# Kernel tuning notes

Hardware: AMD Instinct MI355X
Metric: run time of the kernel (lower is better)

## Reference

```python
import jax, jax.numpy as jnp
import numpy as np

B = 4096
HASH_BITS = 128
TEACHER_DIM = 768
TEMPERATURE = 0.2
CONTRASTIVE_W = 1.0
DISTILL_W = 0.5
QUANT_W = 0.01


def _l2_normalize(x, eps=1e-12):
    # matches torch F.normalize(dim=-1)
    n = jnp.sqrt(jnp.sum(x * x, axis=-1, keepdims=True))
    return x / jnp.maximum(n, eps)


def setup_inputs() -> dict:
    key = jax.random.key(0)
    k1, k2, k3, k4 = jax.random.split(key, 4)
    logits = jax.random.normal(k1, (B, HASH_BITS), dtype=jnp.float32)
    # binary {-1,+1} codes as in the module contract
    hash_codes = jnp.sign(jax.random.normal(k2, (B, HASH_BITS), dtype=jnp.float32))
    hash_codes = jnp.where(hash_codes == 0, 1.0, hash_codes)
    teacher_embed = jax.random.normal(k3, (B, TEACHER_DIM), dtype=jnp.float32)
    # sparse random positives plus self-positives (guarantees each row nonempty)
    rand_pos = jax.random.uniform(k4, (B, B)) < 0.002
    eye = jnp.eye(B, dtype=bool)
    positive_mask = rand_pos | eye
    return {
        "logits": logits,
        "hash_codes": hash_codes,
        "teacher_embed": teacher_embed,
        "positive_mask": positive_mask,
    }


def reference(logits, hash_codes, teacher_embed, positive_mask):
    teacher = _l2_normalize(teacher_embed)

    # ---- contrastive (vectorized form of the per-row python loop) ----
    ln = _l2_normalize(logits)
    sim = (ln @ ln.T) / TEMPERATURE  # [B, B]
    eye = jnp.eye(sim.shape[0], dtype=bool)
    sim_masked = jnp.where(eye, -jnp.inf, sim)
    # per-row stable logsumexp over self-masked similarities
    log_denom = jax.nn.logsumexp(sim_masked, axis=1)  # [B]
    pm = positive_mask.astype(sim.dtype)
    cnt = pm.sum(axis=1)  # [B]
    pos_mean = (sim * pm).sum(axis=1) / jnp.maximum(cnt, 1.0)
    has_pos = cnt > 0
    per_row = jnp.where(has_pos, -pos_mean + log_denom, 0.0)
    num_pos = jnp.maximum(has_pos.sum(), 1)
    loss_cont = per_row.sum() / num_pos.astype(sim.dtype)

    # ---- distillation: hash similarity vs teacher similarity MSE ----
    hash_sim = (hash_codes @ hash_codes.T) / hash_codes.shape[-1]
    teacher_sim = teacher @ teacher.T
    loss_distill = jnp.mean((hash_sim - teacher_sim) ** 2)

    # ---- quantization: push |logits| toward 1 ----
    loss_quant = jnp.mean(jnp.abs(jnp.abs(logits) - 1.0))

    total = (
        CONTRASTIVE_W * loss_cont
        + DISTILL_W * loss_distill
        + QUANT_W * loss_quant
    )
    return total
```

## Files before the change

### kernel.cpp

```cpp
#include <hip/hip_runtime.h>


typedef __bf16 bf16x8 __attribute__((ext_vector_type(8)));
typedef float f32x4 __attribute__((ext_vector_type(4)));

__device__ __forceinline__ unsigned short f2bf(float f) {
  union { float f; unsigned int u; } v; v.f = f;
  unsigned int u = v.u;
  return (unsigned short)((u + 0x7FFFu + ((u >> 16) & 1u)) >> 16);
}

__global__ __launch_bounds__(256) void prep(const float* __restrict__ logits,
                                            const float* __restrict__ hash,
                                            const float* __restrict__ teacher,
                                            unsigned short* __restrict__ P,
                                            unsigned char* __restrict__ Q,
                                            float* __restrict__ qpart,
                                            float* __restrict__ rowexp,
                                            float* __restrict__ possum,
                                            float* __restrict__ cntw,
                                            float* __restrict__ dtot) {
  const int r = blockIdx.x * 4 + (threadIdx.x >> 6);
  const int lane = threadIdx.x & 63;
  float2 tv[6];
  float ss = 0.f;
#pragma unroll
  for (int i = 0; i < 6; ++i) {
    tv[i] = *(const float2*)&teacher[(size_t)r * 768 + i * 128 + 2 * lane];
    ss += tv[i].x * tv[i].x + tv[i].y * tv[i].y;
  }
  const float2 lv = *(const float2*)&logits[(size_t)r * 128 + 2 * lane];
  const float2 hv = *(const float2*)&hash[(size_t)r * 128 + 2 * lane];
  float ssl = lv.x * lv.x + lv.y * lv.y;
  float qv = fabsf(fabsf(lv.x) - 1.f) + fabsf(fabsf(lv.y) - 1.f);
#pragma unroll
  for (int off = 1; off < 64; off <<= 1) {
    ss += __shfl_xor(ss, off, 64);
    ssl += __shfl_xor(ssl, off, 64);
    qv += __shfl_xor(qv, off, 64);
  }
  const float rnt = 11.313708498984761f / fmaxf(sqrtf(ss), 1e-12f);
  const float rnl = 1.f / fmaxf(sqrtf(ssl), 1e-12f);
  unsigned int pb = (unsigned int)f2bf(lv.x * rnl) |
                    ((unsigned int)f2bf(lv.y * rnl) << 16);
  *(unsigned int*)&P[(size_t)r * 128 + 2 * lane] = pb;
  unsigned short hb = (unsigned short)((hv.x >= 0.f ? 0x38 : 0xB8) |
                                       ((hv.y >= 0.f ? 0x38 : 0xB8) << 8));
  *(unsigned short*)&Q[(size_t)r * 896 + 2 * lane] = hb;
#pragma unroll
  for (int i = 0; i < 6; ++i) {
    int p = __builtin_amdgcn_cvt_pk_fp8_f32(tv[i].x * rnt, tv[i].y * rnt, 0, false);
    *(unsigned short*)&Q[(size_t)r * 896 + 128 + i * 128 + 2 * lane] =
        (unsigned short)(p & 0xFFFF);
  }
  if (lane == 0) {
    qpart[r] = qv;
    rowexp[r] = 0.f; possum[r] = 0.f; cntw[r] = 0.f;
    if (r == 0) *dtot = 0.f;
  }
}

#define STAGE_GEN(GA, GB, PITCH)                                               \
  {                                                                            \
    _Pragma("unroll") for (int it = 0; it < 4; ++it) {                         \
      const int task = it * 256 + t;                                           \
      const int row = task >> 3;                                               \
      const int c16 = (task & 7) ^ (row & 7);                                  \
      const unsigned char* gpA = (GA) + (size_t)row * (PITCH) + c16 * 16;      \
      __builtin_amdgcn_global_load_lds(                                        \
          (const __attribute__((address_space(1))) void*)gpA,                  \
          (__attribute__((address_space(3))) void*)&SB[it * 4096 + wave * 1024],\
          16, 0, 0);                                                           \
      if (offdiag) {                                                           \
        const unsigned char* gpB = (GB) + (size_t)row * (PITCH) + c16 * 16;    \
        __builtin_amdgcn_global_load_lds(                                      \
            (const __attribute__((address_space(1))) void*)gpB,                \
            (__attribute__((address_space(3)))                                 \
                 void*)&SB[16384 + it * 4096 + wave * 1024],                   \
            16, 0, 0);                                                         \
      }                                                                        \
    }                                                                          \
  }

#define MFMA_B()                                                               \
  {                                                                            \
    _Pragma("unroll") for (int ks = 0; ks < 2; ++ks) {                         \
      const int ph = ((ks * 4 + qd) ^ (l15 & 7)) * 16;                         \
      bf16x8 af[4], bfr[4];                                                    \
      _Pragma("unroll") for (int rt = 0; rt < 4; ++rt)                         \
          af[rt] = *(const bf16x8*)&SB[(wy * 64 + rt * 16 + l15) * 128 + ph];  \
      _Pragma("unroll") for (int ct = 0; ct < 4; ++ct)                         \
          bfr[ct] = *(const bf16x8*)&SB[boffB +                                \
                                        (wx * 64 + ct * 16 + l15) * 128 + ph]; \
      _Pragma("unroll") for (int rt = 0; rt < 4; ++rt)                         \
          _Pragma("unroll") for (int ct = 0; ct < 4; ++ct) acc[rt][ct] =       \
          __builtin_amdgcn_mfma_f32_16x16x32_bf16(af[rt], bfr[ct],             \
                                                  acc[rt][ct], 0, 0, 0);       \
    }                                                                          \
  }

#define MFMA_Q()                                                               \
  {                                                                            \
    _Pragma("unroll") for (int ks = 0; ks < 4; ++ks) {                         \
      const int g0 = ks * 4 + qd;                                              \
      const int ph = ((g0 >> 1) ^ (l15 & 7)) * 16 + (g0 & 1) * 8;              \
      long af[4], bfr[4];                                                      \
      _Pragma("unroll") for (int rt = 0; rt < 4; ++rt)                         \
          af[rt] = *(const long*)&SB[(wy * 64 + rt * 16 + l15) * 128 + ph];    \
      _Pragma("unroll") for (int ct = 0; ct < 4; ++ct)                         \
          bfr[ct] = *(const long*)&SB[boffB +                                  \
                                      (wx * 64 + ct * 16 + l15) * 128 + ph];   \
      _Pragma("unroll") for (int rt = 0; rt < 4; ++rt)                         \
          _Pragma("unroll") for (int ct = 0; ct < 4; ++ct) acc[rt][ct] =       \
          __builtin_amdgcn_mfma_f32_16x16x32_fp8_fp8(af[rt], bfr[ct],          \
                                                     acc[rt][ct], 0, 0, 0);    \
    }                                                                          \
  }

__global__ __launch_bounds__(256, 3) void mega(const unsigned short* __restrict__ P,
                                               const unsigned char* __restrict__ Q,
                                               const void* __restrict__ mask,
                                               float* __restrict__ rowexp,
                                               float* __restrict__ possum,
                                               float* __restrict__ cntw,
                                               float* __restrict__ dtot) {
  __shared__ __align__(16) unsigned char SB[32768];
  __shared__ float redrow[128][2], redcol[128][2], red4[4];

  const int t = threadIdx.x;
  const int wave = t >> 6, lane = t & 63;
  const int qd = lane >> 4, l15 = lane & 15;
  const int wy = wave >> 1, wx = wave & 1;

  const int b = (int)blockIdx.x;
  const bool isD = (b & 1) == 0;
  const int bb = b >> 1;
  const int l = (bb & 7) * 66 + (bb >> 3);
  int bi = (int)((65.0f - sqrtf(4225.0f - 8.0f * (float)l)) * 0.5f);
  while (bi * (65 - bi) / 2 > l) --bi;
  while ((bi + 1) * (64 - bi) / 2 <= l) ++bi;
  const int bj = bi + (l - bi * (65 - bi) / 2);
  const int ti = bi * 128, tj = bj * 128;
  const bool offdiag = (bi != bj);
  const int boffB = offdiag ? 16384 : 0;

  f32x4 acc[4][4];
#pragma unroll
  for (int rt = 0; rt < 4; ++rt)
#pragma unroll
    for (int ct = 0; ct < 4; ++ct) acc[rt][ct] = {0.f, 0.f, 0.f, 0.f};

  if (isD) {
    const unsigned char* Qa = Q + (size_t)ti * 896;
    const unsigned char* Qb = Q + (size_t)tj * 896;
    for (int kc = 0; kc < 7; ++kc) {
      const int off = (kc < 6) ? (128 + kc * 128) : 0;
      __syncthreads();
      STAGE_GEN(Qa + off, Qb + off, 896);
      __syncthreads();
      if (kc == 6) {
#pragma unroll
        for (int rt = 0; rt < 4; ++rt)
#pragma unroll
          for (int ct = 0; ct < 4; ++ct) acc[rt][ct] = -acc[rt][ct];
      }
      MFMA_Q();
    }
    float dsum = 0.f;
#pragma unroll
    for (int rt = 0; rt < 4; ++rt)
#pragma unroll
      for (int ct = 0; ct < 4; ++ct)
#pragma unroll
        for (int i = 0; i < 4; ++i) dsum += acc[rt][ct][i] * acc[rt][ct][i];
#pragma unroll
    for (int off = 1; off < 64; off <<= 1) dsum += __shfl_xor(dsum, off, 64);
    if (lane == 0) red4[wave] = dsum;
    __syncthreads();
    if (t == 0)
      atomicAdd(dtot, (offdiag ? 2.0f : 1.0f) *
                          (red4[0] + red4[1] + red4[2] + red4[3]));
  } else {
    const unsigned char* Pa = (const unsigned char*)(P + (size_t)ti * 128);
    const unsigned char* Pb = (const unsigned char*)(P + (size_t)tj * 128);
    for (int kc = 0; kc < 2; ++kc) {
      __syncthreads();
      STAGE_GEN(Pa + kc * 128, Pb + kc * 128, 256);
      __syncthreads();
      MFMA_B();
    }

    __syncthreads();
    unsigned char* MD = SB;
    unsigned char* MM = SB + 16384;
    const bool is_byte = ((const unsigned char*)mask)[4097] != 0;
    if (is_byte) {
      const unsigned char* m8d = (const unsigned char*)mask + (size_t)ti * 4096 + tj;
      const unsigned char* m8m = (const unsigned char*)mask + (size_t)tj * 4096 + ti;
#pragma unroll
      for (int it = 0; it < 4; ++it) {
        const int task = it * 256 + t;
        const int row = task >> 3, seg = task & 7;
        __builtin_amdgcn_global_load_lds(
            (const __attribute__((address_space(1))) void*)
                (m8d + (size_t)row * 4096 + seg * 16),
            (__attribute__((address_space(3))) void*)&MD[it * 4096 + wave * 1024],
            16, 0, 0);
        if (offdiag)
          __builtin_amdgcn_global_load_lds(
              (const __attribute__((address_space(1))) void*)
                  (m8m + (size_t)row * 4096 + seg * 16),
              (__attribute__((address_space(3))) void*)&MM[it * 4096 + wave * 1024],
              16, 0, 0);
      }
    } else {
      const unsigned int* m32 = (const unsigned int*)mask;
#pragma unroll
      for (int it = 0; it < 16; ++it) {
        const int task = it * 256 + t;
        const int row = task >> 5, seg = task & 31;
        uint4 v = *(const uint4*)&m32[(size_t)(ti + row) * 4096 + tj + seg * 4];
        uchar4 pk;
        pk.x = v.x ? 1 : 0; pk.y = v.y ? 1 : 0;
        pk.z = v.z ? 1 : 0; pk.w = v.w ? 1 : 0;
        *(uchar4*)&MD[row * 128 + seg * 4] = pk;
        if (offdiag) {
          uint4 w = *(const uint4*)&m32[(size_t)(tj + row) * 4096 + ti + seg * 4];
          uchar4 pm;
          pm.x = w.x ? 1 : 0; pm.y = w.y ? 1 : 0;
          pm.z = w.z ? 1 : 0; pm.w = w.w ? 1 : 0;
          *(uchar4*)&MM[row * 128 + seg * 4] = pm;
        }
      }
    }
    __syncthreads();

    float colp[4] = {0.f, 0.f, 0.f, 0.f};
#pragma unroll
    for (int rt = 0; rt < 4; ++rt) {
#pragma unroll
      for (int r = 0; r < 4; ++r) {
        const int mrow = wy * 64 + rt * 16 + qd * 4 + r;
        const int m = ti + mrow;
        float se = 0.f;
#pragma unroll
        for (int ct = 0; ct < 4; ++ct) {
          const int ncol = wx * 64 + ct * 16 + l15;
          const int n = tj + ncol;
          const float sim = acc[rt][ct][r] * 5.0f;
          const float e = __expf(sim);
          if (offdiag || mrow != ncol) se += e;
          if (offdiag) colp[ct] += e;
          if (MD[mrow * 128 + ncol]) {
            atomicAdd(&possum[m], sim);
            atomicAdd(&cntw[m], 1.0f);
          }
          if (offdiag && MM[ncol * 128 + mrow]) {
            atomicAdd(&possum[n], sim);
            atomicAdd(&cntw[n], 1.0f);
          }
        }
#pragma unroll
        for (int off = 1; off < 16; off <<= 1) se += __shfl_xor(se, off, 64);
        if (l15 == 0) redrow[mrow][wx] = se;
      }
    }
    if (offdiag) {
#pragma unroll
      for (int ct = 0; ct < 4; ++ct) {
        float ce = colp[ct];
        ce += __shfl_xor(ce, 16, 64);
        ce += __shfl_xor(ce, 32, 64);
        if (qd == 0) redcol[wx * 64 + ct * 16 + l15][wy] = ce;
      }
    }
    __syncthreads();
    if (t < 128) {
      atomicAdd(&rowexp[ti + t], redrow[t][0] + redrow[t][1]);
      if (offdiag) atomicAdd(&rowexp[tj + t], redcol[t][0] + redcol[t][1]);
    }
  }
}

__global__ __launch_bounds__(1024) void finalize(const float* __restrict__ rowexp,
                                                 const float* __restrict__ possum,
                                                 const float* __restrict__ cnt,
                                                 const float* __restrict__ qpart,
                                                 const float* __restrict__ dtot,
                                                 float* __restrict__ out) {
  const int t = threadIdx.x;
  const int wave = t >> 6, lane = t & 63;
  float c = 0.f, q = 0.f;
  for (int m = t; m < 4096; m += 1024) {
    c += logf(rowexp[m]) - possum[m] / fmaxf(cnt[m], 1.0f);
    q += qpart[m];
  }
#pragma unroll
  for (int off = 1; off < 64; off <<= 1) {
    c += __shfl_xor(c, off, 64);
    q += __shfl_xor(q, off, 64);
  }
  __shared__ float sc[16], sq[16];
  if (lane == 0) { sc[wave] = c; sq[wave] = q; }
  __syncthreads();
  if (t == 0) {
    float C = 0.f, Q = 0.f;
    for (int i = 0; i < 16; ++i) { C += sc[i]; Q += sq[i]; }
    out[0] = C * (1.0f / 4096.0f) + 0.5f * (dtot[0] * 3.6379788e-12f) +
             0.01f * (Q * (1.0f / 524288.0f));
  }
}

extern "C" void kernel_launch(void* const* d_in, const int* in_sizes, int n_in,
                              void* d_out, int out_size, void* d_ws, size_t ws_size,
                              hipStream_t stream) {
  const float* logits = (const float*)d_in[0];
  const float* hash = (const float*)d_in[1];
  const float* teacher = (const float*)d_in[2];
  const void* mask = d_in[3];
  float* out = (float*)d_out;

  char* ws = (char*)d_ws;
  float* rowexp = (float*)(ws + 0);
  float* possum = (float*)(ws + 16384);
  float* cntw = (float*)(ws + 32768);
  float* qpart = (float*)(ws + 49152);
  float* dtot = (float*)(ws + 65536);
  unsigned short* P = (unsigned short*)(ws + 98304);
  unsigned char* Q = (unsigned char*)(ws + 98304 + 1048576);

  prep<<<1024, 256, 0, stream>>>(logits, hash, teacher, P, Q, qpart, rowexp,
                                 possum, cntw, dtot);
  mega<<<1056, 256, 0, stream>>>(P, Q, mask, rowexp, possum, cntw, dtot);
  finalize<<<1, 1024, 0, stream>>>(rowexp, possum, cntw, qpart, dtot, out);
}
```

Measured before the change: 173.4 us.

## Compute distillation loss through feature-space Gram matrices instead of pairwise similarities

The squared Frobenius norm of the hash-similarity minus teacher-similarity matrix is now computed from the 896x896 Gram matrix of the concatenated fp8 features. Hash-hash and teacher-teacher blocks get a positive sign and cross blocks a negative one. 56 blocks each build one of 28 tile pairs over half of the batch and write fp32 partials. A new small kernel sums the two halves, squares them and accumulates into the total. This cuts distillation FLOPs from O(B²D) to O(BD²) and removes 528 blocks from the main launch. In exchange, operands are gathered byte by byte from LDS, only 56 blocks do the work, and subtracting large norms in fp32 risks cancellation error.

```diff
diff --git a/kernel.cpp b/kernel.cpp
--- a/kernel.cpp
+++ b/kernel.cpp
@@ -99,50 +99,21 @@
     }                                                                          \
   }
 
-#define MFMA_Q()                                                               \
-  {                                                                            \
-    _Pragma("unroll") for (int ks = 0; ks < 4; ++ks) {                         \
-      const int g0 = ks * 4 + qd;                                              \
-      const int ph = ((g0 >> 1) ^ (l15 & 7)) * 16 + (g0 & 1) * 8;              \
-      long af[4], bfr[4];                                                      \
-      _Pragma("unroll") for (int rt = 0; rt < 4; ++rt)                         \
-          af[rt] = *(const long*)&SB[(wy * 64 + rt * 16 + l15) * 128 + ph];    \
-      _Pragma("unroll") for (int ct = 0; ct < 4; ++ct)                         \
-          bfr[ct] = *(const long*)&SB[boffB +                                  \
-                                      (wx * 64 + ct * 16 + l15) * 128 + ph];   \
-      _Pragma("unroll") for (int rt = 0; rt < 4; ++rt)                         \
-          _Pragma("unroll") for (int ct = 0; ct < 4; ++ct) acc[rt][ct] =       \
-          __builtin_amdgcn_mfma_f32_16x16x32_fp8_fp8(af[rt], bfr[ct],          \
-                                                     acc[rt][ct], 0, 0, 0);    \
-    }                                                                          \
-  }
-
 __global__ __launch_bounds__(256, 3) void mega(const unsigned short* __restrict__ P,
                                                const unsigned char* __restrict__ Q,
                                                const void* __restrict__ mask,
                                                float* __restrict__ rowexp,
                                                float* __restrict__ possum,
                                                float* __restrict__ cntw,
-                                               float* __restrict__ dtot) {
+                                               float* __restrict__ Cpart) {
   __shared__ __align__(16) unsigned char SB[32768];
-  __shared__ float redrow[128][2], redcol[128][2], red4[4];
+  __shared__ float redrow[128][2], redcol[128][2];
 
   const int t = threadIdx.x;
   const int wave = t >> 6, lane = t & 63;
   const int qd = lane >> 4, l15 = lane & 15;
   const int wy = wave >> 1, wx = wave & 1;
-
   const int b = (int)blockIdx.x;
-  const bool isD = (b & 1) == 0;
-  const int bb = b >> 1;
-  const int l = (bb & 7) * 66 + (bb >> 3);
-  int bi = (int)((65.0f - sqrtf(4225.0f - 8.0f * (float)l)) * 0.5f);
-  while (bi * (65 - bi) / 2 > l) --bi;
-  while ((bi + 1) * (64 - bi) / 2 <= l) ++bi;
-  const int bj = bi + (l - bi * (65 - bi) / 2);
-  const int ti = bi * 128, tj = bj * 128;
-  const bool offdiag = (bi != bj);
-  const int boffB = offdiag ? 16384 : 0;
 
   f32x4 acc[4][4];
 #pragma unroll
@@ -150,37 +121,74 @@
 #pragma unroll
     for (int ct = 0; ct < 4; ++ct) acc[rt][ct] = {0.f, 0.f, 0.f, 0.f};
 
-  if (isD) {
-    const unsigned char* Qa = Q + (size_t)ti * 896;
-    const unsigned char* Qb = Q + (size_t)tj * 896;
-    for (int kc = 0; kc < 7; ++kc) {
-      const int off = (kc < 6) ? (128 + kc * 128) : 0;
+  if (b < 56) {
+    const int tile = b >> 1, s = b & 1;
+    int I = 0, rem = tile;
+    while (rem >= 7 - I) { rem -= 7 - I; ++I; }
+    const int J = I + rem;
+    const bool offdiag = (I != J);
+    const int boffB = offdiag ? 16384 : 0;
+    const unsigned char* QA = Q + (size_t)s * 2048 * 896 + I * 128;
+    const unsigned char* QB = Q + (size_t)s * 2048 * 896 + J * 128;
+
+    for (int cc = 0; cc < 16; ++cc) {
       __syncthreads();
-      STAGE_GEN(Qa + off, Qb + off, 896);
+      STAGE_GEN(QA + (size_t)cc * 114688, QB + (size_t)cc * 114688, 896);
       __syncthreads();
-      if (kc == 6) {
+#pragma unroll
+      for (int ks = 0; ks < 4; ++ks) {
+        const int ksr = ks * 32 + qd * 8;
+        unsigned long af[4], bfr[4];
+#pragma unroll
+        for (int rt = 0; rt < 4; ++rt) {
+          const int cA = wy * 4 + rt;
+          unsigned long v = 0;
+#pragma unroll
+          for (int j = 0; j < 8; ++j)
+            v |= (unsigned long)SB[(ksr + j) * 128 + ((cA ^ j) << 4) + l15]
+                 << (8 * j);
+          af[rt] = v;
+        }
+#pragma unroll
+        for (int ct = 0; ct < 4; ++ct) {
+          const int cB = wx * 4 + ct;
+          unsigned long v = 0;
+#pragma unroll
+          for (int j = 0; j < 8; ++j)
+            v |= (unsigned long)SB[boffB + (ksr + j) * 128 + ((cB ^ j) << 4) + l15]
+                 << (8 * j);
+          bfr[ct] = v;
+        }
 #pragma unroll
         for (int rt = 0; rt < 4; ++rt)
 #pragma unroll
-          for (int ct = 0; ct < 4; ++ct) acc[rt][ct] = -acc[rt][ct];
-      }
-      MFMA_Q();
-    }
-    float dsum = 0.f;
+          for (int ct = 0; ct < 4; ++ct)
+            acc[rt][ct] = __builtin_amdgcn_mfma_f32_16x16x32_fp8_fp8(
+                (long)af[rt], (long)bfr[ct], acc[rt][ct], 0, 0, 0);
+      }
+    }
+    float* Cp = Cpart + ((size_t)s * 28 + tile) * 16384;
 #pragma unroll
     for (int rt = 0; rt < 4; ++rt)
 #pragma unroll
       for (int ct = 0; ct < 4; ++ct)
 #pragma unroll
-        for (int i = 0; i < 4; ++i) dsum += acc[rt][ct][i] * acc[rt][ct][i];
-#pragma unroll
-    for (int off = 1; off < 64; off <<= 1) dsum += __shfl_xor(dsum, off, 64);
-    if (lane == 0) red4[wave] = dsum;
-    __syncthreads();
-    if (t == 0)
-      atomicAdd(dtot, (offdiag ? 2.0f : 1.0f) *
-                          (red4[0] + red4[1] + red4[2] + red4[3]));
+        for (int r = 0; r < 4; ++r) {
+          const int m = wy * 64 + rt * 16 + qd * 4 + r;
+          const int n = wx * 64 + ct * 16 + l15;
+          Cp[m * 128 + n] = acc[rt][ct][r];
+        }
   } else {
+    const int bb = b - 56;
+    const int l = (bb & 7) * 66 + (bb >> 3);
+    int bi = (int)((65.0f - sqrtf(4225.0f - 8.0f * (float)l)) * 0.5f);
+    while (bi * (65 - bi) / 2 > l) --bi;
+    while ((bi + 1) * (64 - bi) / 2 <= l) ++bi;
+    const int bj = bi + (l - bi * (65 - bi) / 2);
+    const int ti = bi * 128, tj = bj * 128;
+    const bool offdiag = (bi != bj);
+    const int boffB = offdiag ? 16384 : 0;
+
     const unsigned char* Pa = (const unsigned char*)(P + (size_t)ti * 128);
     const unsigned char* Pb = (const unsigned char*)(P + (size_t)tj * 128);
     for (int kc = 0; kc < 2; ++kc) {
@@ -282,6 +290,29 @@
   }
 }
 
+__global__ __launch_bounds__(256) void gsq(const float* __restrict__ Cpart,
+                                           float* __restrict__ dtot) {
+  const int tile = blockIdx.x;
+  int I = 0, rem = tile;
+  while (rem >= 7 - I) { rem -= 7 - I; ++I; }
+  const int J = I + rem;
+  const float mult = (I == J ? 1.f : 2.f) * (((I == 0) == (J == 0)) ? 1.f : -1.f);
+  const float* a = Cpart + (size_t)tile * 16384;
+  const float* bpt = Cpart + (size_t)(28 + tile) * 16384;
+  const int t = threadIdx.x;
+  float ssum = 0.f;
+  for (int i = t; i < 16384; i += 256) {
+    const float c = a[i] + bpt[i];
+    ssum += c * c;
+  }
+#pragma unroll
+  for (int off = 1; off < 64; off <<= 1) ssum += __shfl_xor(ssum, off, 64);
+  __shared__ float sred[4];
+  if ((t & 63) == 0) sred[t >> 6] = ssum;
+  __syncthreads();
+  if (t == 0) atomicAdd(dtot, mult * (sred[0] + sred[1] + sred[2] + sred[3]));
+}
+
 __global__ __launch_bounds__(1024) void finalize(const float* __restrict__ rowexp,
                                                  const float* __restrict__ possum,
                                                  const float* __restrict__ cnt,
@@ -328,9 +359,11 @@
   float* dtot = (float*)(ws + 65536);
   unsigned short* P = (unsigned short*)(ws + 98304);
   unsigned char* Q = (unsigned char*)(ws + 98304 + 1048576);
+  float* Cpart = (float*)(ws + 4816896);
 
   prep<<<1024, 256, 0, stream>>>(logits, hash, teacher, P, Q, qpart, rowexp,
                                  possum, cntw, dtot);
-  mega<<<1056, 256, 0, stream>>>(P, Q, mask, rowexp, possum, cntw, dtot);
+  mega<<<584, 256, 0, stream>>>(P, Q, mask, rowexp, possum, cntw, Cpart);
+  gsq<<<28, 256, 0, stream>>>(Cpart, dtot);
   finalize<<<1, 1024, 0, stream>>>(rowexp, possum, cntw, qpart, dtot, out);
 }
```

New measurement: 198.4 us. +14.4%, slower.

## Compute distillation loss via transposed Gram matrices and full-grid contrastive tiles

Applied to the files above, without the earlier changes.

Rewrites the distillation MSE using the identity ||AAᵀ−BBᵀ||² = ||[A;B]ᵀ[A;B]||-style Gram products over the feature dimension. Prep now writes a transposed fp8 matrix (896×4096), and 28 blocks compute the 7×7 upper-triangular feature Gram blocks with K=4096, instead of forming 4096×4096 similarity tiles. The contrastive part drops triangular symmetry and uses all 1024 tiles, which removes the transposed mask loads and the column atomics. Risks: prep now runs on only 32 blocks with byte-wise LDS transposes, and the long-K fp8 accumulations may lose accuracy.

```diff
diff --git a/kernel.cpp b/kernel.cpp
--- a/kernel.cpp
+++ b/kernel.cpp
@@ -14,49 +14,80 @@
                                             const float* __restrict__ hash,
                                             const float* __restrict__ teacher,
                                             unsigned short* __restrict__ P,
-                                            unsigned char* __restrict__ Q,
+                                            unsigned char* __restrict__ QT,
                                             float* __restrict__ qpart,
                                             float* __restrict__ rowexp,
                                             float* __restrict__ possum,
                                             float* __restrict__ cntw,
                                             float* __restrict__ dtot) {
-  const int r = blockIdx.x * 4 + (threadIdx.x >> 6);
-  const int lane = threadIdx.x & 63;
-  float2 tv[6];
-  float ss = 0.f;
-#pragma unroll
-  for (int i = 0; i < 6; ++i) {
-    tv[i] = *(const float2*)&teacher[(size_t)r * 768 + i * 128 + 2 * lane];
-    ss += tv[i].x * tv[i].x + tv[i].y * tv[i].y;
-  }
-  const float2 lv = *(const float2*)&logits[(size_t)r * 128 + 2 * lane];
-  const float2 hv = *(const float2*)&hash[(size_t)r * 128 + 2 * lane];
-  float ssl = lv.x * lv.x + lv.y * lv.y;
-  float qv = fabsf(fabsf(lv.x) - 1.f) + fabsf(fabsf(lv.y) - 1.f);
-#pragma unroll
-  for (int off = 1; off < 64; off <<= 1) {
-    ss += __shfl_xor(ss, off, 64);
-    ssl += __shfl_xor(ssl, off, 64);
-    qv += __shfl_xor(qv, off, 64);
-  }
-  const float rnt = 11.313708498984761f / fmaxf(sqrtf(ss), 1e-12f);
-  const float rnl = 1.f / fmaxf(sqrtf(ssl), 1e-12f);
-  unsigned int pb = (unsigned int)f2bf(lv.x * rnl) |
-                    ((unsigned int)f2bf(lv.y * rnl) << 16);
-  *(unsigned int*)&P[(size_t)r * 128 + 2 * lane] = pb;
-  unsigned short hb = (unsigned short)((hv.x >= 0.f ? 0x38 : 0xB8) |
-                                       ((hv.y >= 0.f ? 0x38 : 0xB8) << 8));
-  *(unsigned short*)&Q[(size_t)r * 896 + 2 * lane] = hb;
-#pragma unroll
-  for (int i = 0; i < 6; ++i) {
-    int p = __builtin_amdgcn_cvt_pk_fp8_f32(tv[i].x * rnt, tv[i].y * rnt, 0, false);
-    *(unsigned short*)&Q[(size_t)r * 896 + 128 + i * 128 + 2 * lane] =
-        (unsigned short)(p & 0xFFFF);
-  }
-  if (lane == 0) {
-    qpart[r] = qv;
-    rowexp[r] = 0.f; possum[r] = 0.f; cntw[r] = 0.f;
-    if (r == 0) *dtot = 0.f;
+  __shared__ float rnt[128];
+  __shared__ unsigned char QL[128 * 129];
+  const int t = threadIdx.x, wave = t >> 6, lane = t & 63;
+  const int r0 = (int)blockIdx.x * 128;
+
+  for (int rr = 0; rr < 32; ++rr) {
+    const int rl = wave * 32 + rr, r = r0 + rl;
+    float ss = 0.f;
+#pragma unroll
+    for (int i = 0; i < 12; ++i) {
+      const float v = teacher[(size_t)r * 768 + i * 64 + lane];
+      ss += v * v;
+    }
+    const float l0 = logits[(size_t)r * 128 + lane];
+    const float l1 = logits[(size_t)r * 128 + 64 + lane];
+    float ssl = l0 * l0 + l1 * l1;
+    float qv = fabsf(fabsf(l0) - 1.f) + fabsf(fabsf(l1) - 1.f);
+#pragma unroll
+    for (int off = 1; off < 64; off <<= 1) {
+      ss += __shfl_xor(ss, off, 64);
+      ssl += __shfl_xor(ssl, off, 64);
+      qv += __shfl_xor(qv, off, 64);
+    }
+    const float rnl = 1.f / fmaxf(sqrtf(ssl), 1e-12f);
+    P[(size_t)r * 128 + lane] = f2bf(l0 * rnl);
+    P[(size_t)r * 128 + 64 + lane] = f2bf(l1 * rnl);
+    if (lane == 0) {
+      rnt[rl] = 11.313708498984761f / fmaxf(sqrtf(ss), 1e-12f);
+      qpart[r] = qv;
+    }
+  }
+  if (t < 128) { rowexp[r0 + t] = 0.f; possum[r0 + t] = 0.f; cntw[r0 + t] = 0.f; }
+  if (blockIdx.x == 0 && t == 0) *dtot = 0.f;
+  __syncthreads();
+
+  for (int g = 0; g < 7; ++g) {
+    const int rB = t >> 5, cB = (t & 31) * 4;
+    for (int pass = 0; pass < 16; ++pass) {
+      const int r = rB + pass * 8;
+      if (g == 0) {
+        const float4 v = *(const float4*)&hash[(size_t)(r0 + r) * 128 + cB];
+        QL[r * 129 + cB + 0] = v.x >= 0.f ? 0x38 : 0xB8;
+        QL[r * 129 + cB + 1] = v.y >= 0.f ? 0x38 : 0xB8;
+        QL[r * 129 + cB + 2] = v.z >= 0.f ? 0x38 : 0xB8;
+        QL[r * 129 + cB + 3] = v.w >= 0.f ? 0x38 : 0xB8;
+      } else {
+        const float sc = rnt[r];
+        const float4 v =
+            *(const float4*)&teacher[(size_t)(r0 + r) * 768 + (g - 1) * 128 + cB];
+        float vv[4] = {v.x * sc, v.y * sc, v.z * sc, v.w * sc};
+#pragma unroll
+        for (int k = 0; k < 4; ++k) {
+          const int p8 = __builtin_amdgcn_cvt_pk_fp8_f32(vv[k], vv[k], 0, false);
+          QL[r * 129 + cB + k] = (unsigned char)(p8 & 0xFF);
+        }
+      }
+    }
+    __syncthreads();
+#pragma unroll
+    for (int i = 0; i < 4; ++i) {
+      const int idx = t + 256 * i;
+      const int cl = idx >> 3, seg = idx & 7;
+      unsigned char buf[16];
+#pragma unroll
+      for (int j = 0; j < 16; ++j) buf[j] = QL[(seg * 16 + j) * 129 + cl];
+      *(uint4*)&QT[(size_t)(g * 128 + cl) * 4096 + r0 + seg * 16] = *(uint4*)buf;
+    }
+    __syncthreads();
   }
 }
 
@@ -118,31 +149,20 @@
   }
 
 __global__ __launch_bounds__(256, 3) void mega(const unsigned short* __restrict__ P,
-                                               const unsigned char* __restrict__ Q,
+                                               const unsigned char* __restrict__ QT,
                                                const void* __restrict__ mask,
                                                float* __restrict__ rowexp,
                                                float* __restrict__ possum,
                                                float* __restrict__ cntw,
                                                float* __restrict__ dtot) {
   __shared__ __align__(16) unsigned char SB[32768];
-  __shared__ float redrow[128][2], redcol[128][2], red4[4];
+  __shared__ float redrow[128][2], red4[4];
 
   const int t = threadIdx.x;
   const int wave = t >> 6, lane = t & 63;
   const int qd = lane >> 4, l15 = lane & 15;
   const int wy = wave >> 1, wx = wave & 1;
-
   const int b = (int)blockIdx.x;
-  const bool isD = (b & 1) == 0;
-  const int bb = b >> 1;
-  const int l = (bb & 7) * 66 + (bb >> 3);
-  int bi = (int)((65.0f - sqrtf(4225.0f - 8.0f * (float)l)) * 0.5f);
-  while (bi * (65 - bi) / 2 > l) --bi;
-  while ((bi + 1) * (64 - bi) / 2 <= l) ++bi;
-  const int bj = bi + (l - bi * (65 - bi) / 2);
-  const int ti = bi * 128, tj = bj * 128;
-  const bool offdiag = (bi != bj);
-  const int boffB = offdiag ? 16384 : 0;
 
   f32x4 acc[4][4];
 #pragma unroll
@@ -150,20 +170,18 @@
 #pragma unroll
     for (int ct = 0; ct < 4; ++ct) acc[rt][ct] = {0.f, 0.f, 0.f, 0.f};
 
-  if (isD) {
-    const unsigned char* Qa = Q + (size_t)ti * 896;
-    const unsigned char* Qb = Q + (size_t)tj * 896;
-    for (int kc = 0; kc < 7; ++kc) {
-      const int off = (kc < 6) ? (128 + kc * 128) : 0;
+  if (b < 28) {
+    int I = 0, rem = b;
+    while (rem >= 7 - I) { rem -= 7 - I; ++I; }
+    const int J = I + rem;
+    const bool offdiag = (I != J);
+    const int boffB = offdiag ? 16384 : 0;
+    const unsigned char* QA = QT + (size_t)I * 128 * 4096;
+    const unsigned char* QB = QT + (size_t)J * 128 * 4096;
+    for (int kc = 0; kc < 32; ++kc) {
       __syncthreads();
-      STAGE_GEN(Qa + off, Qb + off, 896);
+      STAGE_GEN(QA + kc * 128, QB + kc * 128, 4096);
       __syncthreads();
-      if (kc == 6) {
-#pragma unroll
-        for (int rt = 0; rt < 4; ++rt)
-#pragma unroll
-          for (int ct = 0; ct < 4; ++ct) acc[rt][ct] = -acc[rt][ct];
-      }
       MFMA_Q();
     }
     float dsum = 0.f;
@@ -177,10 +195,19 @@
     for (int off = 1; off < 64; off <<= 1) dsum += __shfl_xor(dsum, off, 64);
     if (lane == 0) red4[wave] = dsum;
     __syncthreads();
-    if (t == 0)
-      atomicAdd(dtot, (offdiag ? 2.0f : 1.0f) *
-                          (red4[0] + red4[1] + red4[2] + red4[3]));
+    if (t == 0) {
+      const float mult = (I == J ? 1.f : 2.f) *
+                         (((I == 0) == (J == 0)) ? 1.f : -1.f);
+      atomicAdd(dtot, mult * (red4[0] + red4[1] + red4[2] + red4[3]));
+    }
   } else {
+    const int bb = b - 28;
+    const int l = (bb & 7) * 128 + (bb >> 3);
+    const int bi = l >> 5, bj = l & 31;
+    const int ti = bi * 128, tj = bj * 128;
+    const bool offdiag = (bi != bj);
+    const int boffB = offdiag ? 16384 : 0;
+
     const unsigned char* Pa = (const unsigned char*)(P + (size_t)ti * 128);
     const unsigned char* Pb = (const unsigned char*)(P + (size_t)tj * 128);
     for (int kc = 0; kc < 2; ++kc) {
@@ -192,11 +219,9 @@
 
     __syncthreads();
     unsigned char* MD = SB;
-    unsigned char* MM = SB + 16384;
     const bool is_byte = ((const unsigned char*)mask)[4097] != 0;
     if (is_byte) {
       const unsigned char* m8d = (const unsigned char*)mask + (size_t)ti * 4096 + tj;
-      const unsigned char* m8m = (const unsigned char*)mask + (size_t)tj * 4096 + ti;
 #pragma unroll
       for (int it = 0; it < 4; ++it) {
         const int task = it * 256 + t;
@@ -206,12 +231,6 @@
                 (m8d + (size_t)row * 4096 + seg * 16),
             (__attribute__((address_space(3))) void*)&MD[it * 4096 + wave * 1024],
             16, 0, 0);
-        if (offdiag)
-          __builtin_amdgcn_global_load_lds(
-              (const __attribute__((address_space(1))) void*)
-                  (m8m + (size_t)row * 4096 + seg * 16),
-              (__attribute__((address_space(3))) void*)&MM[it * 4096 + wave * 1024],
-              16, 0, 0);
       }
     } else {
       const unsigned int* m32 = (const unsigned int*)mask;
@@ -219,23 +238,15 @@
       for (int it = 0; it < 16; ++it) {
         const int task = it * 256 + t;
         const int row = task >> 5, seg = task & 31;
-        uint4 v = *(const uint4*)&m32[(size_t)(ti + row) * 4096 + tj + seg * 4];
+        const uint4 v = *(const uint4*)&m32[(size_t)(ti + row) * 4096 + tj + seg * 4];
         uchar4 pk;
         pk.x = v.x ? 1 : 0; pk.y = v.y ? 1 : 0;
         pk.z = v.z ? 1 : 0; pk.w = v.w ? 1 : 0;
         *(uchar4*)&MD[row * 128 + seg * 4] = pk;
-        if (offdiag) {
-          uint4 w = *(const uint4*)&m32[(size_t)(tj + row) * 4096 + ti + seg * 4];
-          uchar4 pm;
-          pm.x = w.x ? 1 : 0; pm.y = w.y ? 1 : 0;
-          pm.z = w.z ? 1 : 0; pm.w = w.w ? 1 : 0;
-          *(uchar4*)&MM[row * 128 + seg * 4] = pm;
-        }
       }
     }
     __syncthreads();
 
-    float colp[4] = {0.f, 0.f, 0.f, 0.f};
 #pragma unroll
     for (int rt = 0; rt < 4; ++rt) {
 #pragma unroll
@@ -249,36 +260,19 @@
           const int n = tj + ncol;
           const float sim = acc[rt][ct][r] * 5.0f;
           const float e = __expf(sim);
-          if (offdiag || mrow != ncol) se += e;
-          if (offdiag) colp[ct] += e;
+          if (m != n) se += e;
           if (MD[mrow * 128 + ncol]) {
             atomicAdd(&possum[m], sim);
             atomicAdd(&cntw[m], 1.0f);
           }
-          if (offdiag && MM[ncol * 128 + mrow]) {
-            atomicAdd(&possum[n], sim);
-            atomicAdd(&cntw[n], 1.0f);
-          }
         }
 #pragma unroll
         for (int off = 1; off < 16; off <<= 1) se += __shfl_xor(se, off, 64);
         if (l15 == 0) redrow[mrow][wx] = se;
       }
     }
-    if (offdiag) {
-#pragma unroll
-      for (int ct = 0; ct < 4; ++ct) {
-        float ce = colp[ct];
-        ce += __shfl_xor(ce, 16, 64);
-        ce += __shfl_xor(ce, 32, 64);
-        if (qd == 0) redcol[wx * 64 + ct * 16 + l15][wy] = ce;
-      }
-    }
-    __syncthreads();
-    if (t < 128) {
-      atomicAdd(&rowexp[ti + t], redrow[t][0] + redrow[t][1]);
-      if (offdiag) atomicAdd(&rowexp[tj + t], redcol[t][0] + redcol[t][1]);
-    }
+    __syncthreads();
+    if (t < 128) atomicAdd(&rowexp[ti + t], redrow[t][0] + redrow[t][1]);
   }
 }
 
@@ -327,10 +321,10 @@
   float* qpart = (float*)(ws + 49152);
   float* dtot = (float*)(ws + 65536);
   unsigned short* P = (unsigned short*)(ws + 98304);
-  unsigned char* Q = (unsigned char*)(ws + 98304 + 1048576);
-
-  prep<<<1024, 256, 0, stream>>>(logits, hash, teacher, P, Q, qpart, rowexp,
-                                 possum, cntw, dtot);
-  mega<<<1056, 256, 0, stream>>>(P, Q, mask, rowexp, possum, cntw, dtot);
+  unsigned char* QT = (unsigned char*)(ws + 98304 + 1048576);
+
+  prep<<<32, 256, 0, stream>>>(logits, hash, teacher, P, QT, qpart, rowexp,
+                               possum, cntw, dtot);
+  mega<<<1052, 256, 0, stream>>>(P, QT, mask, rowexp, possum, cntw, dtot);
   finalize<<<1, 1024, 0, stream>>>(rowexp, possum, cntw, qpart, dtot, out);
 }
```

Result: slower. 199.7 us (+15.1%).
